# Kernel tuning notes

Measured on AMD Instinct MI355X. Metric: run time of the kernel, lower is better.

## Reference

```python
import jax, jax.numpy as jnp
import numpy as np

N = 100000
E = 1600000
BN_EPS = 1e-5


def setup_inputs() -> dict:
    key = jax.random.key(0)
    ks = jax.random.split(key, 12)
    d = 128
    s = 1.0 / np.sqrt(d)
    inp = {
        "x": jax.random.normal(ks[0], (N, d), jnp.float32),
        "x_importance": jax.random.uniform(ks[1], (N, 1), jnp.float32),
        "edge_index": jax.random.randint(ks[2], (2, E), 0, N, jnp.int64),
        "bn_gamma": jnp.ones((d,), jnp.float32),
        "bn_beta": jnp.zeros((d,), jnp.float32),
        "Wfc": jax.random.normal(ks[3], (d, d), jnp.float32) * s,
    }
    for i in range(1, 6):
        inp[f"W{i}"] = jax.random.normal(ks[3 + i], (d, d), jnp.float32) * s
        inp[f"b{i}"] = jnp.zeros((d,), jnp.float32)
    return inp


def reference(x, x_importance, edge_index, bn_gamma, bn_beta,
              W1, b1, W2, b2, W3, b3, W4, b4, W5, b5, Wfc):
    src, dst = edge_index[0], edge_index[1]

    # bn_in (training-mode batch stats over nodes)
    h = x * x_importance
    mean = jnp.mean(h, axis=0)
    var = jnp.mean(jnp.square(h - mean), axis=0)  # biased, as torch BN normalize
    h = (h - mean) * jax.lax.rsqrt(var + BN_EPS) * bn_gamma + bn_beta

    def gin_conv(h, W, b):
        # GINConv with eps=0: nn(h + sum_{j in N(i)} h_j)
        agg = jax.ops.segment_sum(h[src], dst, num_segments=N)  # [N, d]
        return jnp.tanh((h + agg) @ W + b)

    xs = []
    for W, b in ((W1, b1), (W2, b2), (W3, b3), (W4, b4), (W5, b5)):
        h = gin_conv(h, W, b)
        xs.append(h)
    xs.append(jnp.tanh(h @ Wfc))
    return jnp.concatenate(xs, axis=-1)  # [N, 5*dim + out_channels]
```

## Files before the change

### kernel.cpp

```cpp
#include <hip/hip_runtime.h>
#include <hip/hip_fp16.h>
#include <cstdint>
#include <cstddef>

#define DIM 128
#define BN_EPS_ 1e-5f

typedef _Float16 half8 __attribute__((ext_vector_type(8)));
typedef float floatx4 __attribute__((ext_vector_type(4)));
typedef short shortx8 __attribute__((ext_vector_type(8)));

#define SCALE_H 32768.f
#define INV_H   (1.f/32768.f)

__device__ __forceinline__ float fast_tanh(float x) {
    float t = __expf(2.f * x);
    return 1.f - 2.f / (t + 1.f);
}

__device__ __forceinline__ short quant(float v, float scale) {
    int q = __float2int_rn(v * scale);
    q = max(min(q, 32767), -32767);
    return (short)q;
}

__global__ __launch_bounds__(256) void k_mul_stats(
    const float* __restrict__ x, const float* __restrict__ imp,
    float* __restrict__ gsum, float* __restrict__ gsq, int N)
{
    __shared__ float ls[256], lq[256];
    int t = threadIdx.x;
    int f = t & 127;
    int rs = t >> 7;
    float s = 0.f, q = 0.f;
    for (int r = blockIdx.x * 2 + rs; r < N; r += gridDim.x * 2) {
        float v = x[(size_t)r * DIM + f] * imp[r];
        s += v; q += v * v;
    }
    ls[t] = s; lq[t] = q;
    __syncthreads();
    if (t < 128) {
        atomicAdd(&gsum[f], ls[t] + ls[t + 128]);
        atomicAdd(&gsq[f],  lq[t] + lq[t + 128]);
    }
}

__global__ void k_finalize(const float* __restrict__ gsum, const float* __restrict__ gsq,
                           const float* __restrict__ gamma, const float* __restrict__ beta,
                           float* __restrict__ scale, float* __restrict__ shift, int N)
{
    int f = threadIdx.x;
    float mean = gsum[f] / (float)N;
    float var  = gsq[f] / (float)N - mean * mean;
    var = fmaxf(var, 0.f);
    float sc = gamma[f] * rsqrtf(var + BN_EPS_);
    scale[f] = sc;
    shift[f] = beta[f] - mean * sc;
}

__global__ __launch_bounds__(256) void k_bn_apply(
    const float* __restrict__ x, const float* __restrict__ imp,
    const float* __restrict__ scale, const float* __restrict__ shift,
    float* __restrict__ h0, int n32)
{
    int i = blockIdx.x * 256 + threadIdx.x;
    if (i >= n32) return;
    int r = i >> 5, f4 = i & 31;
    float im = imp[r];
    float4 v  = ((const float4*)x)[i];
    float4 sc = ((const float4*)scale)[f4];
    float4 sh = ((const float4*)shift)[f4];
    float4 o;
    o.x = fmaf(v.x * im, sc.x, sh.x);
    o.y = fmaf(v.y * im, sc.y, sh.y);
    o.z = fmaf(v.z * im, sc.z, sh.z);
    o.w = fmaf(v.w * im, sc.w, sh.w);
    ((float4*)h0)[i] = o;
}

__global__ __launch_bounds__(256) void k_wsplit(const float* __restrict__ W,
                                               _Float16* __restrict__ WtHi,
                                               _Float16* __restrict__ WtLo)
{
    for (int e = blockIdx.x * 256 + threadIdx.x; e < DIM * DIM; e += gridDim.x * 256) {
        int k = e >> 7, n = e & 127;
        float w = W[e];
        _Float16 hi = (_Float16)w;
        _Float16 lo = (_Float16)(w - (float)hi);
        WtHi[n * DIM + k] = hi;
        WtLo[n * DIM + k] = lo;
    }
}

__global__ void k_hist(const int* __restrict__ dst, int* __restrict__ deg, int E)
{
    int e = blockIdx.x * 256 + threadIdx.x;
    if (e < E) atomicAdd(&deg[dst[e]], 1);
}

__global__ __launch_bounds__(256) void k_chunksum(const int* __restrict__ deg, int* __restrict__ csum, int N)
{
    __shared__ int s[256];
    int t = threadIdx.x;
    int i = blockIdx.x * 256 + t;
    s[t] = (i < N) ? deg[i] : 0;
    __syncthreads();
    for (int off = 128; off > 0; off >>= 1) {
        if (t < off) s[t] += s[t + off];
        __syncthreads();
    }
    if (t == 0) csum[blockIdx.x] = s[0];
}

__global__ void k_scanchunks(int* __restrict__ csum, int* __restrict__ rstart, int nchunks, int N)
{
    __shared__ int s[512];
    int t = threadIdx.x;
    s[t] = (t < nchunks) ? csum[t] : 0;
    __syncthreads();
    for (int off = 1; off < 512; off <<= 1) {
        int add = (t >= off) ? s[t - off] : 0;
        __syncthreads();
        s[t] += add;
        __syncthreads();
    }
    if (t < nchunks) csum[t] = (t > 0) ? s[t - 1] : 0;
    if (t == 511) rstart[N] = s[511];
}

__global__ __launch_bounds__(256) void k_scanwithin(
    const int* __restrict__ deg, const int* __restrict__ csum,
    int* __restrict__ rstart, int* __restrict__ cursor, int N)
{
    __shared__ int s[256];
    int t = threadIdx.x;
    int i = blockIdx.x * 256 + t;
    int v = (i < N) ? deg[i] : 0;
    s[t] = v;
    __syncthreads();
    for (int off = 1; off < 256; off <<= 1) {
        int add = (t >= off) ? s[t - off] : 0;
        __syncthreads();
        s[t] += add;
        __syncthreads();
    }
    if (i < N) {
        int rs = csum[blockIdx.x] + s[t] - v;
        rstart[i] = rs;
        cursor[i] = rs;
    }
}

__global__ void k_scatter(const int* __restrict__ src, const int* __restrict__ dst,
                          int* __restrict__ cursor, int* __restrict__ csr, int E)
{
    int e = blockIdx.x * 256 + threadIdx.x;
    if (e < E) {
        int d = dst[e];
        int pos = atomicAdd(&cursor[d], 1);
        csr[pos] = src[e];
    }
}

__global__ __launch_bounds__(256) void k_aggF(
    const float* __restrict__ h0,
    const int* __restrict__ rstart, const int* __restrict__ csr,
    float* __restrict__ S, int N)
{
    int node = blockIdx.x * 8 + (threadIdx.x >> 5);
    if (node >= N) return;
    int lane = threadIdx.x & 31;
    int beg = rstart[node], end = rstart[node + 1];

    float4 s = *(const float4*)(h0 + (size_t)node * DIM + lane * 4);
    int e = beg;
    for (; e + 2 <= end; e += 2) {
        int n0 = csr[e], n1 = csr[e + 1];
        float4 a = *(const float4*)(h0 + (size_t)n0 * DIM + lane * 4);
        float4 b = *(const float4*)(h0 + (size_t)n1 * DIM + lane * 4);
        s.x += a.x + b.x; s.y += a.y + b.y;
        s.z += a.z + b.z; s.w += a.w + b.w;
    }
    if (e < end) {
        float4 a = *(const float4*)(h0 + (size_t)csr[e] * DIM + lane * 4);
        s.x += a.x; s.y += a.y; s.z += a.z; s.w += a.w;
    }
    *(float4*)(S + (size_t)node * DIM + lane * 4) = s;
}

__global__ __launch_bounds__(256) void k_aggS(
    const short* __restrict__ hq,
    const int* __restrict__ rstart, const int* __restrict__ csr,
    float* __restrict__ S, float invScale, int N)
{
    int node = blockIdx.x * 16 + (threadIdx.x >> 4);
    if (node >= N) return;
    int l16 = threadIdx.x & 15;
    const shortx8* base = (const shortx8*)hq;

    int beg = rstart[node], end = rstart[node + 1];

    shortx8 sv = base[(size_t)node * 16 + l16];
    int acc[8];
#pragma unroll
    for (int j = 0; j < 8; ++j) acc[j] = (int)sv[j];

    int e = beg;
    for (; e + 4 <= end; e += 4) {
        int n0 = csr[e], n1 = csr[e + 1], n2 = csr[e + 2], n3 = csr[e + 3];
        shortx8 v0 = base[(size_t)n0 * 16 + l16];
        shortx8 v1 = base[(size_t)n1 * 16 + l16];
        shortx8 v2 = base[(size_t)n2 * 16 + l16];
        shortx8 v3 = base[(size_t)n3 * 16 + l16];
#pragma unroll
        for (int j = 0; j < 8; ++j)
            acc[j] += ((int)v0[j] + (int)v1[j]) + ((int)v2[j] + (int)v3[j]);
    }
    for (; e < end; ++e) {
        shortx8 v0 = base[(size_t)csr[e] * 16 + l16];
#pragma unroll
        for (int j = 0; j < 8; ++j) acc[j] += (int)v0[j];
    }

    float4 o0, o1;
    o0.x = acc[0] * invScale; o0.y = acc[1] * invScale;
    o0.z = acc[2] * invScale; o0.w = acc[3] * invScale;
    o1.x = acc[4] * invScale; o1.y = acc[5] * invScale;
    o1.z = acc[6] * invScale; o1.w = acc[7] * invScale;
    float* dp = S + (size_t)node * DIM + l16 * 8;
    *(float4*)dp = o0;
    *(float4*)(dp + 4) = o1;
}

__global__ __launch_bounds__(256) void k_gemmT(
    const float* __restrict__ A, int lda,
    const _Float16* __restrict__ WtHi, const _Float16* __restrict__ WtLo,
    const float* __restrict__ bias,
    float* __restrict__ outSlice,
    short* __restrict__ hqNext,
    int N)
{
    int wave = threadIdx.x >> 6;
    int lane = threadIdx.x & 63;
    int r0 = blockIdx.x * 64 + wave * 16;
    int arow = r0 + (lane & 15);
    if (arow >= N) arow = N - 1;
    int kg = (lane >> 4) * 8;

    half8 ahi[4], alo[4];
#pragma unroll
    for (int ks = 0; ks < 4; ++ks) {
        const float* ap = A + (size_t)arow * lda + ks * 32 + kg;
        float4 f0 = *(const float4*)ap;
        float4 f1 = *(const float4*)(ap + 4);
        float fv[8] = {f0.x, f0.y, f0.z, f0.w, f1.x, f1.y, f1.z, f1.w};
#pragma unroll
        for (int j = 0; j < 8; ++j) {
            _Float16 h = (_Float16)fv[j];
            ahi[ks][j] = h;
            alo[ks][j] = (_Float16)(fv[j] - (float)h);
        }
    }

    floatx4 acc[8];
#pragma unroll
    for (int nt = 0; nt < 8; ++nt) acc[nt] = (floatx4){0.f, 0.f, 0.f, 0.f};

#pragma unroll
    for (int nt = 0; nt < 8; ++nt) {
        int ncol = nt * 16 + (lane & 15);
#pragma unroll
        for (int ks = 0; ks < 4; ++ks) {
            half8 bhi = *(const half8*)(WtHi + (size_t)ncol * DIM + ks * 32 + kg);
            half8 blo = *(const half8*)(WtLo + (size_t)ncol * DIM + ks * 32 + kg);
            acc[nt] = __builtin_amdgcn_mfma_f32_16x16x32_f16(ahi[ks], bhi, acc[nt], 0, 0, 0);
            acc[nt] = __builtin_amdgcn_mfma_f32_16x16x32_f16(alo[ks], bhi, acc[nt], 0, 0, 0);
            acc[nt] = __builtin_amdgcn_mfma_f32_16x16x32_f16(ahi[ks], blo, acc[nt], 0, 0, 0);
        }
    }

    int rbase = r0 + (lane >> 4) * 4;
#pragma unroll
    for (int nt = 0; nt < 8; ++nt) {
        int col = nt * 16 + (lane & 15);
        float bv = bias ? bias[col] : 0.f;
#pragma unroll
        for (int j = 0; j < 4; ++j) {
            int r = rbase + j;
            if (r < N) {
                float t = fast_tanh(acc[nt][j] + bv);
                outSlice[(size_t)r * 768 + col] = t;
                if (hqNext) hqNext[(size_t)r * DIM + col] = quant(t, SCALE_H);
            }
        }
    }
}

extern "C" void kernel_launch(void* const* d_in, const int* in_sizes, int n_in,
                              void* d_out, int out_size, void* d_ws, size_t ws_size,
                              hipStream_t stream)
{
    const float* x     = (const float*)d_in[0];
    const float* imp   = (const float*)d_in[1];
    const int*   eidx  = (const int*)d_in[2];
    const float* gamma = (const float*)d_in[3];
    const float* beta  = (const float*)d_in[4];
    const float* Wfc   = (const float*)d_in[5];
    const float* W[5]; const float* B[5];
    for (int i = 0; i < 5; ++i) {
        W[i] = (const float*)d_in[6 + 2 * i];
        B[i] = (const float*)d_in[7 + 2 * i];
    }
    float* out = (float*)d_out;

    const int N = in_sizes[0] / DIM;
    const int E = in_sizes[2] / 2;
    const int* src = eidx;
    const int* dst = eidx + E;

    char* ws = (char*)d_ws;
    size_t off = 0;
    auto alloc = [&](size_t b) -> char* {
        char* p = ws + off;
        off = (off + b + 255) & ~(size_t)255;
        return p;
    };
    float* h0     = (float*)alloc((size_t)N * DIM * 4);
    short* hq     = (short*)alloc((size_t)N * DIM * 2);
    float* S      = (float*)alloc((size_t)N * DIM * 4);
    _Float16* WtHi[6]; _Float16* WtLo[6];
    for (int i = 0; i < 6; ++i) {
        WtHi[i] = (_Float16*)alloc(DIM * DIM * 2);
        WtLo[i] = (_Float16*)alloc(DIM * DIM * 2);
    }
    int*   deg    = (int*)alloc((size_t)N * 4);
    int*   rstart = (int*)alloc((size_t)(N + 1) * 4);
    int*   cursor = (int*)alloc((size_t)N * 4);
    int*   csr    = (int*)alloc((size_t)E * 4);
    float* gsum   = (float*)alloc(128 * 4);
    float* gsq    = (float*)alloc(128 * 4);
    float* scale  = (float*)alloc(128 * 4);
    float* shift  = (float*)alloc(128 * 4);
    int*   csum   = (int*)alloc(4096 * 4);

    hipMemsetAsync(gsum, 0, 128 * 4, stream);
    hipMemsetAsync(gsq, 0, 128 * 4, stream);
    hipMemsetAsync(deg, 0, (size_t)N * 4, stream);

    k_mul_stats<<<1024, 256, 0, stream>>>(x, imp, gsum, gsq, N);
    k_finalize<<<1, 128, 0, stream>>>(gsum, gsq, gamma, beta, scale, shift, N);
    k_bn_apply<<<(N * 32 + 255) / 256, 256, 0, stream>>>(x, imp, scale, shift, h0, N * 32);

    k_hist<<<(E + 255) / 256, 256, 0, stream>>>(dst, deg, E);
    int nchunks = (N + 255) / 256;
    k_chunksum<<<nchunks, 256, 0, stream>>>(deg, csum, N);
    k_scanchunks<<<1, 512, 0, stream>>>(csum, rstart, nchunks, N);
    k_scanwithin<<<nchunks, 256, 0, stream>>>(deg, csum, rstart, cursor, N);
    k_scatter<<<(E + 255) / 256, 256, 0, stream>>>(src, dst, cursor, csr, E);

    for (int i = 0; i < 5; ++i)
        k_wsplit<<<8, 256, 0, stream>>>(W[i], WtHi[i], WtLo[i]);
    k_wsplit<<<8, 256, 0, stream>>>(Wfc, WtHi[5], WtLo[5]);

    k_aggF<<<(N + 7) / 8, 256, 0, stream>>>(h0, rstart, csr, S, N);
    k_gemmT<<<(N + 63) / 64, 256, 0, stream>>>(S, DIM, WtHi[0], WtLo[0], B[0],
                                               out, hq, N);
    for (int l = 1; l < 5; ++l) {
        k_aggS<<<(N + 15) / 16, 256, 0, stream>>>(hq, rstart, csr, S, INV_H, N);
        k_gemmT<<<(N + 63) / 64, 256, 0, stream>>>(S, DIM, WtHi[l], WtLo[l], B[l],
                                                   out + (size_t)l * DIM,
                                                   (l < 4) ? hq : nullptr, N);
    }
    k_gemmT<<<(N + 63) / 64, 256, 0, stream>>>(out + (size_t)4 * DIM, 768,
                                               WtHi[5], WtLo[5], nullptr,
                                               out + (size_t)5 * DIM, nullptr, N);
}
```

Measured before the change: 1.161 ms.

## Fuse aggregation with GEMM per layer and quantize BN output to int16

Each GIN layer now gathers neighbour features into shared memory and runs the MFMA GEMM in the same kernel, so the fp32 aggregate buffer is no longer written and read back through global memory. The batch-norm output is quantized to int16 with a dynamic scale computed from per-feature max magnitudes, which lets the first layer use the cheaper 16-bit gather instead of fp32. The final Wfc GEMM is fused into the last layer kernel and reuses the tanh outputs from shared memory. The cost is heavier per-block shared memory and register use, which may lower occupancy during the gather phase, and extra quantization error on the first layer's input.

```diff
diff --git a/kernel.cpp b/kernel.cpp
--- a/kernel.cpp
+++ b/kernel.cpp
@@ -24,58 +24,76 @@
     return (short)q;
 }
 
-__global__ __launch_bounds__(256) void k_mul_stats(
+__global__ __launch_bounds__(256) void k_stats(
     const float* __restrict__ x, const float* __restrict__ imp,
-    float* __restrict__ gsum, float* __restrict__ gsq, int N)
-{
-    __shared__ float ls[256], lq[256];
+    float* __restrict__ gsum, float* __restrict__ gsq, float* __restrict__ gmax, int N)
+{
+    __shared__ float ls[256], lq[256], lm[256];
     int t = threadIdx.x;
     int f = t & 127;
     int rs = t >> 7;
-    float s = 0.f, q = 0.f;
+    float s = 0.f, q = 0.f, m = 0.f;
     for (int r = blockIdx.x * 2 + rs; r < N; r += gridDim.x * 2) {
         float v = x[(size_t)r * DIM + f] * imp[r];
-        s += v; q += v * v;
-    }
-    ls[t] = s; lq[t] = q;
+        s += v; q += v * v; m = fmaxf(m, fabsf(v));
+    }
+    ls[t] = s; lq[t] = q; lm[t] = m;
     __syncthreads();
     if (t < 128) {
         atomicAdd(&gsum[f], ls[t] + ls[t + 128]);
         atomicAdd(&gsq[f],  lq[t] + lq[t + 128]);
+        float mm = fmaxf(lm[t], lm[t + 128]);
+        atomicMax((int*)&gmax[f], __float_as_int(mm));
     }
 }
 
 __global__ void k_finalize(const float* __restrict__ gsum, const float* __restrict__ gsq,
+                           const float* __restrict__ gmax,
                            const float* __restrict__ gamma, const float* __restrict__ beta,
-                           float* __restrict__ scale, float* __restrict__ shift, int N)
-{
+                           float* __restrict__ scale, float* __restrict__ shift,
+                           float* __restrict__ q0, int N)
+{
+    __shared__ float sb[128];
     int f = threadIdx.x;
     float mean = gsum[f] / (float)N;
     float var  = gsq[f] / (float)N - mean * mean;
     var = fmaxf(var, 0.f);
     float sc = gamma[f] * rsqrtf(var + BN_EPS_);
+    float sh = beta[f] - mean * sc;
     scale[f] = sc;
-    shift[f] = beta[f] - mean * sc;
-}
-
-__global__ __launch_bounds__(256) void k_bn_apply(
+    shift[f] = sh;
+    sb[f] = fabsf(sc) * gmax[f] + fabsf(sh);
+    __syncthreads();
+    for (int off = 64; off > 0; off >>= 1) {
+        if (f < off) sb[f] = fmaxf(sb[f], sb[f + off]);
+        __syncthreads();
+    }
+    if (f == 0) {
+        float Q = fmaxf(sb[0], 1e-20f);
+        q0[0] = 32766.f / Q;
+        q0[1] = Q / 32766.f;
+    }
+}
+
+__global__ __launch_bounds__(256) void k_bn_quant(
     const float* __restrict__ x, const float* __restrict__ imp,
     const float* __restrict__ scale, const float* __restrict__ shift,
-    float* __restrict__ h0, int n32)
+    const float* __restrict__ q0, short* __restrict__ hq0, int n32)
 {
     int i = blockIdx.x * 256 + threadIdx.x;
     if (i >= n32) return;
+    float qs = q0[0];
     int r = i >> 5, f4 = i & 31;
     float im = imp[r];
     float4 v  = ((const float4*)x)[i];
     float4 sc = ((const float4*)scale)[f4];
     float4 sh = ((const float4*)shift)[f4];
-    float4 o;
-    o.x = fmaf(v.x * im, sc.x, sh.x);
-    o.y = fmaf(v.y * im, sc.y, sh.y);
-    o.z = fmaf(v.z * im, sc.z, sh.z);
-    o.w = fmaf(v.w * im, sc.w, sh.w);
-    ((float4*)h0)[i] = o;
+    short q[4];
+    q[0] = quant(fmaf(v.x * im, sc.x, sh.x), qs);
+    q[1] = quant(fmaf(v.y * im, sc.y, sh.y), qs);
+    q[2] = quant(fmaf(v.z * im, sc.z, sh.z), qs);
+    q[3] = quant(fmaf(v.w * im, sc.w, sh.w), qs);
+    *(float2*)(hq0 + (size_t)i * 4) = *(float2*)q;
 }
 
 __global__ __launch_bounds__(256) void k_wsplit(const float* __restrict__ W,
@@ -162,97 +180,74 @@
     }
 }
 
-__global__ __launch_bounds__(256) void k_aggF(
-    const float* __restrict__ h0,
+template<int FINAL>
+__global__ __launch_bounds__(256) void k_layer(
+    const short* __restrict__ hqIn,
     const int* __restrict__ rstart, const int* __restrict__ csr,
-    float* __restrict__ S, int N)
-{
-    int node = blockIdx.x * 8 + (threadIdx.x >> 5);
-    if (node >= N) return;
-    int lane = threadIdx.x & 31;
-    int beg = rstart[node], end = rstart[node + 1];
-
-    float4 s = *(const float4*)(h0 + (size_t)node * DIM + lane * 4);
-    int e = beg;
-    for (; e + 2 <= end; e += 2) {
-        int n0 = csr[e], n1 = csr[e + 1];
-        float4 a = *(const float4*)(h0 + (size_t)n0 * DIM + lane * 4);
-        float4 b = *(const float4*)(h0 + (size_t)n1 * DIM + lane * 4);
-        s.x += a.x + b.x; s.y += a.y + b.y;
-        s.z += a.z + b.z; s.w += a.w + b.w;
-    }
-    if (e < end) {
-        float4 a = *(const float4*)(h0 + (size_t)csr[e] * DIM + lane * 4);
-        s.x += a.x; s.y += a.y; s.z += a.z; s.w += a.w;
-    }
-    *(float4*)(S + (size_t)node * DIM + lane * 4) = s;
-}
-
-__global__ __launch_bounds__(256) void k_aggS(
-    const short* __restrict__ hq,
-    const int* __restrict__ rstart, const int* __restrict__ csr,
-    float* __restrict__ S, float invScale, int N)
-{
-    int node = blockIdx.x * 16 + (threadIdx.x >> 4);
-    if (node >= N) return;
-    int l16 = threadIdx.x & 15;
-    const shortx8* base = (const shortx8*)hq;
-
-    int beg = rstart[node], end = rstart[node + 1];
-
-    shortx8 sv = base[(size_t)node * 16 + l16];
-    int acc[8];
-#pragma unroll
-    for (int j = 0; j < 8; ++j) acc[j] = (int)sv[j];
-
-    int e = beg;
-    for (; e + 4 <= end; e += 4) {
-        int n0 = csr[e], n1 = csr[e + 1], n2 = csr[e + 2], n3 = csr[e + 3];
-        shortx8 v0 = base[(size_t)n0 * 16 + l16];
-        shortx8 v1 = base[(size_t)n1 * 16 + l16];
-        shortx8 v2 = base[(size_t)n2 * 16 + l16];
-        shortx8 v3 = base[(size_t)n3 * 16 + l16];
-#pragma unroll
-        for (int j = 0; j < 8; ++j)
-            acc[j] += ((int)v0[j] + (int)v1[j]) + ((int)v2[j] + (int)v3[j]);
-    }
-    for (; e < end; ++e) {
-        shortx8 v0 = base[(size_t)csr[e] * 16 + l16];
-#pragma unroll
-        for (int j = 0; j < 8; ++j) acc[j] += (int)v0[j];
-    }
-
-    float4 o0, o1;
-    o0.x = acc[0] * invScale; o0.y = acc[1] * invScale;
-    o0.z = acc[2] * invScale; o0.w = acc[3] * invScale;
-    o1.x = acc[4] * invScale; o1.y = acc[5] * invScale;
-    o1.z = acc[6] * invScale; o1.w = acc[7] * invScale;
-    float* dp = S + (size_t)node * DIM + l16 * 8;
-    *(float4*)dp = o0;
-    *(float4*)(dp + 4) = o1;
-}
-
-__global__ __launch_bounds__(256) void k_gemmT(
-    const float* __restrict__ A, int lda,
+    const float* __restrict__ invPtr, float invConst,
     const _Float16* __restrict__ WtHi, const _Float16* __restrict__ WtLo,
     const float* __restrict__ bias,
-    float* __restrict__ outSlice,
-    short* __restrict__ hqNext,
+    const _Float16* __restrict__ WfHi, const _Float16* __restrict__ WfLo,
+    float* __restrict__ outS,
+    float* __restrict__ outF,
+    short* __restrict__ hqOut,
     int N)
 {
-    int wave = threadIdx.x >> 6;
-    int lane = threadIdx.x & 63;
-    int r0 = blockIdx.x * 64 + wave * 16;
-    int arow = r0 + (lane & 15);
-    if (arow >= N) arow = N - 1;
+    __shared__ float sA[64][132];
+    int t = threadIdx.x;
+    float inv = invPtr ? invPtr[0] : invConst;
+
+    {
+        int l16 = t & 15;
+        int sg  = t >> 4;
+        const shortx8* base = (const shortx8*)hqIn;
+#pragma unroll
+        for (int pass = 0; pass < 4; ++pass) {
+            int nl = pass * 16 + sg;
+            int node = blockIdx.x * 64 + nl;
+            float* dstp = &sA[nl][l16 * 8];
+            if (node < N) {
+                int beg = rstart[node], end = rstart[node + 1];
+                shortx8 sv = base[(size_t)node * 16 + l16];
+                int acc[8];
+#pragma unroll
+                for (int j = 0; j < 8; ++j) acc[j] = (int)sv[j];
+                int e = beg;
+                for (; e + 4 <= end; e += 4) {
+                    int n0 = csr[e], n1 = csr[e + 1], n2 = csr[e + 2], n3 = csr[e + 3];
+                    shortx8 v0 = base[(size_t)n0 * 16 + l16];
+                    shortx8 v1 = base[(size_t)n1 * 16 + l16];
+                    shortx8 v2 = base[(size_t)n2 * 16 + l16];
+                    shortx8 v3 = base[(size_t)n3 * 16 + l16];
+#pragma unroll
+                    for (int j = 0; j < 8; ++j)
+                        acc[j] += ((int)v0[j] + (int)v1[j]) + ((int)v2[j] + (int)v3[j]);
+                }
+                for (; e < end; ++e) {
+                    shortx8 v0 = base[(size_t)csr[e] * 16 + l16];
+#pragma unroll
+                    for (int j = 0; j < 8; ++j) acc[j] += (int)v0[j];
+                }
+#pragma unroll
+                for (int j = 0; j < 8; ++j) dstp[j] = acc[j] * inv;
+            } else {
+#pragma unroll
+                for (int j = 0; j < 8; ++j) dstp[j] = 0.f;
+            }
+        }
+    }
+    __syncthreads();
+
+    int wave = t >> 6;
+    int lane = t & 63;
     int kg = (lane >> 4) * 8;
+    int arowL = wave * 16 + (lane & 15);
 
     half8 ahi[4], alo[4];
 #pragma unroll
     for (int ks = 0; ks < 4; ++ks) {
-        const float* ap = A + (size_t)arow * lda + ks * 32 + kg;
-        float4 f0 = *(const float4*)ap;
-        float4 f1 = *(const float4*)(ap + 4);
+        float4 f0 = *(const float4*)&sA[arowL][ks * 32 + kg];
+        float4 f1 = *(const float4*)&sA[arowL][ks * 32 + kg + 4];
         float fv[8] = {f0.x, f0.y, f0.z, f0.w, f1.x, f1.y, f1.z, f1.w};
 #pragma unroll
         for (int j = 0; j < 8; ++j) {
@@ -265,7 +260,6 @@
     floatx4 acc[8];
 #pragma unroll
     for (int nt = 0; nt < 8; ++nt) acc[nt] = (floatx4){0.f, 0.f, 0.f, 0.f};
-
 #pragma unroll
     for (int nt = 0; nt < 8; ++nt) {
         int ncol = nt * 16 + (lane & 15);
@@ -279,18 +273,71 @@
         }
     }
 
-    int rbase = r0 + (lane >> 4) * 4;
+    int rbaseL = wave * 16 + (lane >> 4) * 4;
+    int rglob = blockIdx.x * 64 + rbaseL;
+    float tv[8][4];
 #pragma unroll
     for (int nt = 0; nt < 8; ++nt) {
         int col = nt * 16 + (lane & 15);
-        float bv = bias ? bias[col] : 0.f;
+        float bv = bias[col];
 #pragma unroll
         for (int j = 0; j < 4; ++j) {
-            int r = rbase + j;
+            float tt = fast_tanh(acc[nt][j] + bv);
+            tv[nt][j] = tt;
+            int r = rglob + j;
             if (r < N) {
-                float t = fast_tanh(acc[nt][j] + bv);
-                outSlice[(size_t)r * 768 + col] = t;
-                if (hqNext) hqNext[(size_t)r * DIM + col] = quant(t, SCALE_H);
+                outS[(size_t)r * 768 + col] = tt;
+                if (hqOut) hqOut[(size_t)r * DIM + col] = quant(tt, SCALE_H);
+            }
+        }
+    }
+
+    if (FINAL) {
+        __syncthreads();
+#pragma unroll
+        for (int nt = 0; nt < 8; ++nt) {
+            int col = nt * 16 + (lane & 15);
+#pragma unroll
+            for (int j = 0; j < 4; ++j)
+                sA[rbaseL + j][col] = tv[nt][j];
+        }
+        __syncthreads();
+
+        half8 chi[4], clo[4];
+#pragma unroll
+        for (int ks = 0; ks < 4; ++ks) {
+            float4 f0 = *(const float4*)&sA[arowL][ks * 32 + kg];
+            float4 f1 = *(const float4*)&sA[arowL][ks * 32 + kg + 4];
+            float fv[8] = {f0.x, f0.y, f0.z, f0.w, f1.x, f1.y, f1.z, f1.w};
+#pragma unroll
+            for (int j = 0; j < 8; ++j) {
+                _Float16 h = (_Float16)fv[j];
+                chi[ks][j] = h;
+                clo[ks][j] = (_Float16)(fv[j] - (float)h);
+            }
+        }
+        floatx4 ac2[8];
+#pragma unroll
+        for (int nt = 0; nt < 8; ++nt) ac2[nt] = (floatx4){0.f, 0.f, 0.f, 0.f};
+#pragma unroll
+        for (int nt = 0; nt < 8; ++nt) {
+            int ncol = nt * 16 + (lane & 15);
+#pragma unroll
+            for (int ks = 0; ks < 4; ++ks) {
+                half8 bhi = *(const half8*)(WfHi + (size_t)ncol * DIM + ks * 32 + kg);
+                half8 blo = *(const half8*)(WfLo + (size_t)ncol * DIM + ks * 32 + kg);
+                ac2[nt] = __builtin_amdgcn_mfma_f32_16x16x32_f16(chi[ks], bhi, ac2[nt], 0, 0, 0);
+                ac2[nt] = __builtin_amdgcn_mfma_f32_16x16x32_f16(clo[ks], bhi, ac2[nt], 0, 0, 0);
+                ac2[nt] = __builtin_amdgcn_mfma_f32_16x16x32_f16(chi[ks], blo, ac2[nt], 0, 0, 0);
+            }
+        }
+#pragma unroll
+        for (int nt = 0; nt < 8; ++nt) {
+            int col = nt * 16 + (lane & 15);
+#pragma unroll
+            for (int j = 0; j < 4; ++j) {
+                int r = rglob + j;
+                if (r < N) outF[(size_t)r * 768 + col] = fast_tanh(ac2[nt][j]);
             }
         }
     }
@@ -325,9 +372,8 @@
         off = (off + b + 255) & ~(size_t)255;
         return p;
     };
-    float* h0     = (float*)alloc((size_t)N * DIM * 4);
-    short* hq     = (short*)alloc((size_t)N * DIM * 2);
-    float* S      = (float*)alloc((size_t)N * DIM * 4);
+    short* hqA = (short*)alloc((size_t)N * DIM * 2);
+    short* hqB = (short*)alloc((size_t)N * DIM * 2);
     _Float16* WtHi[6]; _Float16* WtLo[6];
     for (int i = 0; i < 6; ++i) {
         WtHi[i] = (_Float16*)alloc(DIM * DIM * 2);
@@ -339,17 +385,20 @@
     int*   csr    = (int*)alloc((size_t)E * 4);
     float* gsum   = (float*)alloc(128 * 4);
     float* gsq    = (float*)alloc(128 * 4);
+    float* gmax   = (float*)alloc(128 * 4);
     float* scale  = (float*)alloc(128 * 4);
     float* shift  = (float*)alloc(128 * 4);
+    float* q0     = (float*)alloc(2 * 4);
     int*   csum   = (int*)alloc(4096 * 4);
 
     hipMemsetAsync(gsum, 0, 128 * 4, stream);
-    hipMemsetAsync(gsq, 0, 128 * 4, stream);
-    hipMemsetAsync(deg, 0, (size_t)N * 4, stream);
-
-    k_mul_stats<<<1024, 256, 0, stream>>>(x, imp, gsum, gsq, N);
-    k_finalize<<<1, 128, 0, stream>>>(gsum, gsq, gamma, beta, scale, shift, N);
-    k_bn_apply<<<(N * 32 + 255) / 256, 256, 0, stream>>>(x, imp, scale, shift, h0, N * 32);
+    hipMemsetAsync(gsq,  0, 128 * 4, stream);
+    hipMemsetAsync(gmax, 0, 128 * 4, stream);
+    hipMemsetAsync(deg,  0, (size_t)N * 4, stream);
+
+    k_stats<<<1024, 256, 0, stream>>>(x, imp, gsum, gsq, gmax, N);
+    k_finalize<<<1, 128, 0, stream>>>(gsum, gsq, gmax, gamma, beta, scale, shift, q0, N);
+    k_bn_quant<<<(N * 32 + 255) / 256, 256, 0, stream>>>(x, imp, scale, shift, q0, hqA, N * 32);
 
     k_hist<<<(E + 255) / 256, 256, 0, stream>>>(dst, deg, E);
     int nchunks = (N + 255) / 256;
@@ -362,16 +411,18 @@
         k_wsplit<<<8, 256, 0, stream>>>(W[i], WtHi[i], WtLo[i]);
     k_wsplit<<<8, 256, 0, stream>>>(Wfc, WtHi[5], WtLo[5]);
 
-    k_aggF<<<(N + 7) / 8, 256, 0, stream>>>(h0, rstart, csr, S, N);
-    k_gemmT<<<(N + 63) / 64, 256, 0, stream>>>(S, DIM, WtHi[0], WtLo[0], B[0],
-                                               out, hq, N);
-    for (int l = 1; l < 5; ++l) {
-        k_aggS<<<(N + 15) / 16, 256, 0, stream>>>(hq, rstart, csr, S, INV_H, N);
-        k_gemmT<<<(N + 63) / 64, 256, 0, stream>>>(S, DIM, WtHi[l], WtLo[l], B[l],
-                                                   out + (size_t)l * DIM,
-                                                   (l < 4) ? hq : nullptr, N);
-    }
-    k_gemmT<<<(N + 63) / 64, 256, 0, stream>>>(out + (size_t)4 * DIM, 768,
-                                               WtHi[5], WtLo[5], nullptr,
-                                               out + (size_t)5 * DIM, nullptr, N);
-}
+    int grid = (N + 63) / 64;
+    short* cur = hqA;
+    short* nxt = hqB;
+    for (int l = 0; l < 4; ++l) {
+        k_layer<0><<<grid, 256, 0, stream>>>(cur, rstart, csr,
+            (l == 0) ? (q0 + 1) : nullptr, INV_H,
+            WtHi[l], WtLo[l], B[l], nullptr, nullptr,
+            out + (size_t)l * DIM, nullptr, nxt, N);
+        short* tmp = cur; cur = nxt; nxt = tmp;
+    }
+    k_layer<1><<<grid, 256, 0, stream>>>(cur, rstart, csr,
+        nullptr, INV_H,
+        WtHi[4], WtLo[4], B[4], WtHi[5], WtLo[5],
+        out + (size_t)4 * DIM, out + (size_t)5 * DIM, nullptr, N);
+}
```

Result: faster. 1.030 ms (-11.3%).
